# Kernel tuning notes

Hardware: AMD Instinct MI355X
Metric: run time of the kernel (lower is better)

## Reference

```python
import jax, jax.numpy as jnp
import numpy as np

N = 200000      # nodes
E = 1600000     # edges
B = 1000        # graphs
SD = 64         # state_dim
AD = 32         # action_dim
H = 128         # HIDDEN_LAYER
EPS = 1e-5


def setup_inputs() -> dict:
    key = jax.random.key(0)
    ks = jax.random.split(key, 16)
    x = jax.random.normal(ks[0], (N, SD), dtype=jnp.float32)
    action = jax.random.normal(ks[1], (N, AD), dtype=jnp.float32)
    edge_index = jax.random.randint(ks[2], (2, E), 0, N, dtype=jnp.int64)
    batch_size = jnp.sort(jax.random.randint(ks[3], (N,), 0, B, dtype=jnp.int64))
    # parameters (Linear weights stored [in, out]; torch init std=0.1 for fc layers)
    W_gcn = jax.random.normal(ks[4], (SD, H), dtype=jnp.float32) / np.sqrt(SD)
    b_gcn = jnp.zeros((H,), jnp.float32)
    g0 = jnp.ones((H,), jnp.float32); be0 = jnp.zeros((H,), jnp.float32)
    W1 = jax.random.normal(ks[5], (H, H), dtype=jnp.float32) * 0.1
    b1 = jnp.zeros((H,), jnp.float32)
    g1 = jnp.ones((H,), jnp.float32); be1 = jnp.zeros((H,), jnp.float32)
    W2 = jax.random.normal(ks[6], (AD, H), dtype=jnp.float32) * 0.1
    b2 = jnp.zeros((H,), jnp.float32)
    g2 = jnp.ones((H,), jnp.float32); be2 = jnp.zeros((H,), jnp.float32)
    W3 = jax.random.normal(ks[7], (2 * H, 1), dtype=jnp.float32) * 0.1
    b3 = jnp.zeros((1,), jnp.float32)
    return dict(x=x, action=action, W_gcn=W_gcn, b_gcn=b_gcn, g0=g0, be0=be0,
                W1=W1, b1=b1, g1=g1, be1=be1, W2=W2, b2=b2, g2=g2, be2=be2,
                W3=W3, b3=b3, edge_index=edge_index, batch_size=batch_size)


def _bn(h, gamma, beta):
    # BatchNorm1d, training-mode batch statistics over the node axis
    mu = jnp.mean(h, axis=0)
    var = jnp.var(h, axis=0)
    return (h - mu) * jax.lax.rsqrt(var + EPS) * gamma + beta


def _gcn(x, edge_index, W, b):
    # GCN conv with self-loops and symmetric normalization:
    # out_i = sum_{j in N(i) u {i}} (d_i d_j)^{-1/2} (x_j W) + b
    loops = jnp.arange(N, dtype=edge_index.dtype)
    src = jnp.concatenate([edge_index[0], loops])
    dst = jnp.concatenate([edge_index[1], loops])
    deg = jax.ops.segment_sum(jnp.ones_like(dst, dtype=x.dtype), dst, num_segments=N)
    dinv = jax.lax.rsqrt(deg)                       # deg >= 1 due to self-loops
    norm = dinv[src] * dinv[dst]                    # [E+N]
    xw = x @ W                                      # [N, H]
    msg = xw[src] * norm[:, None]                   # [E+N, H]
    return jax.ops.segment_sum(msg, dst, num_segments=N) + b


def reference(x, action, W_gcn, b_gcn, g0, be0, W1, b1, g1, be1,
              W2, b2, g2, be2, W3, b3, edge_index, batch_size):
    h0 = jax.nn.relu(_gcn(x, edge_index, W_gcn, b_gcn))
    h0n = _bn(h0, g0, be0)
    h1 = jax.nn.relu(h0n @ W1 + b1)
    h1n = _bn(h1, g1, be1)
    h2 = jax.nn.relu(action @ W2 + b2)
    h2n = _bn(h2, g2, be2)
    feat = jnp.concatenate([h1n, h2n], axis=1)      # [N, 2H]
    sums = jax.ops.segment_sum(feat, batch_size, num_segments=B)
    cnts = jax.ops.segment_sum(jnp.ones((N,), feat.dtype), batch_size, num_segments=B)
    pooled = sums / jnp.maximum(cnts, 1.0)[:, None]  # [B, 2H]
    return pooled @ W3 + b3                          # [B, 1]
```

## Files before the change

kernel.cpp:

```cpp
#include <hip/hip_runtime.h>

typedef unsigned short u16;
typedef unsigned int   u32;
typedef __bf16 bf16x8 __attribute__((ext_vector_type(8)));
typedef float  f32x4  __attribute__((ext_vector_type(4)));

#define EPS 1e-5f
#define BSHIFT 9

__device__ __forceinline__ float b2f(u16 u){ union{u32 i; float f;} v; v.i=((u32)u)<<16; return v.f; }
__device__ __forceinline__ u16 f2b(float f){
  u32 x = __float_as_uint(f);
  u32 r = x + 0x7fffu + ((x>>16)&1u);
  return (u16)(r>>16);
}

template<int K, bool RELU, bool HASBIAS, bool AF32, bool POOL>
__global__ __launch_bounds__(256, 3) void k_gemm(const void* __restrict__ Av,
                                                 const u16* __restrict__ BhiT,
                                                 const u16* __restrict__ BloT,
                                                 const float* __restrict__ bias,
                                                 u16* __restrict__ C,
                                                 float* __restrict__ stats,
                                                 const int* __restrict__ batch,
                                                 float* __restrict__ P, int M)
{
  constexpr int KM = K / 8;
  constexpr int KR = K / 32;
  __shared__ u16 lds[2 * 64 * K];
  __shared__ float sred[64], qred[64];
  const int tid = threadIdx.x;
  const int ch = blockIdx.x & 1;
  for (int i = tid; i < 64 * KM; i += 256) {
    const int n = i / KM, kb = i % KM;
    const int kb2 = kb ^ (n & (KM - 1));
    const int gsrc = ((ch * 64 + n) * KM + kb) * 8;
    *(uint4*)(&lds[(n * KM + kb2) * 8])          = *(const uint4*)(BhiT + gsrc);
    *(uint4*)(&lds[64 * K + (n * KM + kb2) * 8]) = *(const uint4*)(BloT + gsrc);
  }
  if (tid < 64) { sred[tid] = 0.f; qred[tid] = 0.f; }
  __syncthreads();
  const int wid = tid >> 6, lane = tid & 63, q = lane >> 4, r16 = lane & 15;
  const int ntiles = M >> 6;
  const int t0 = blockIdx.x >> 1, tstride = gridDim.x >> 1;
  float ls[4], lq[4];
#pragma unroll
  for (int nb = 0; nb < 4; nb++) { ls[nb] = 0.f; lq[nb] = 0.f; }
  float bv[4];
#pragma unroll
  for (int nb = 0; nb < 4; nb++) bv[nb] = HASBIAS ? bias[ch * 64 + nb * 16 + r16] : 0.f;

  bf16x8 av[KR];
  bf16x8 avn[KR];
  f32x4  fx0[KR], fx1[KR];
  int bgc[4], bgn[4];

  auto issueA = [&](int tile) {
    const int arow = (tile << 6) + (wid << 4) + r16;
    if (AF32) {
      const float* Af = (const float*)Av + (size_t)arow * K + q * 8;
#pragma unroll
      for (int kk = 0; kk < KR; kk++) {
        fx0[kk] = *(const f32x4*)(Af + kk * 32);
        fx1[kk] = *(const f32x4*)(Af + kk * 32 + 4);
      }
    } else {
      const u16* Ab = (const u16*)Av + (size_t)arow * K + q * 8;
#pragma unroll
      for (int kk = 0; kk < KR; kk++) avn[kk] = *(const bf16x8*)(Ab + kk * 32);
    }
    if (POOL) {
      const int rbase = (tile << 6) + (wid << 4) + (q << 2);
#pragma unroll
      for (int r = 0; r < 4; r++) bgn[r] = batch[rbase + r];
    }
  };
  auto commitA = [&]() {
    if (AF32) {
#pragma unroll
      for (int kk = 0; kk < KR; kk++)
#pragma unroll
        for (int j = 0; j < 4; j++) { av[kk][j] = (__bf16)fx0[kk][j]; av[kk][4 + j] = (__bf16)fx1[kk][j]; }
    } else {
#pragma unroll
      for (int kk = 0; kk < KR; kk++) av[kk] = avn[kk];
    }
    if (POOL) {
#pragma unroll
      for (int r = 0; r < 4; r++) bgc[r] = bgn[r];
    }
  };

  if (t0 < ntiles) issueA(t0);
  for (int tile = t0; tile < ntiles; tile += tstride) {
    commitA();
    const int nxt = tile + tstride;
    if (nxt < ntiles) issueA(nxt);

    f32x4 acc[4];
#pragma unroll
    for (int nb = 0; nb < 4; nb++) acc[nb] = (f32x4){0.f, 0.f, 0.f, 0.f};
#pragma unroll
    for (int kk = 0; kk < KR; kk++) {
#pragma unroll
      for (int nb = 0; nb < 4; nb++) {
        const int n = nb * 16 + r16;
        const int kb2 = (kk * 4 + q) ^ (n & (KM - 1));
        const bf16x8 bh = *(const bf16x8*)(&lds[(n * KM + kb2) * 8]);
        const bf16x8 bl = *(const bf16x8*)(&lds[64 * K + (n * KM + kb2) * 8]);
        acc[nb] = __builtin_amdgcn_mfma_f32_16x16x32_bf16(av[kk], bh, acc[nb], 0, 0, 0);
        acc[nb] = __builtin_amdgcn_mfma_f32_16x16x32_bf16(av[kk], bl, acc[nb], 0, 0, 0);
      }
    }

    const int rbase = (tile << 6) + (wid << 4) + (q << 2);
#pragma unroll
    for (int nb = 0; nb < 4; nb++) {
      const int col = ch * 64 + nb * 16 + r16;
#pragma unroll
      for (int r = 0; r < 4; r++) {
        float v = acc[nb][r] + bv[nb];
        if (RELU) v = fmaxf(v, 0.f);
        ls[nb] += v; lq[nb] += v * v;
        if (!POOL) C[(size_t)(rbase + r) * 128 + col] = f2b(v);
        else acc[nb][r] = v;
      }
    }
    if (POOL) {
      const int g0 = __shfl(bgc[0], 0, 64);
      const int g1 = __shfl(bgc[3], 48, 64);
      for (int g = g0; g <= g1; ++g) {
#pragma unroll
        for (int nb = 0; nb < 4; nb++) {
          float sv = 0.f;
#pragma unroll
          for (int r = 0; r < 4; r++) sv += (bgc[r] == g) ? acc[nb][r] : 0.f;
          sv += __shfl_xor(sv, 16, 64);
          sv += __shfl_xor(sv, 32, 64);
          if (q == 0) atomicAdd(&P[g * 128 + ch * 64 + nb * 16 + r16], sv);
        }
      }
    }
  }
#pragma unroll
  for (int nb = 0; nb < 4; nb++) {
    atomicAdd(&sred[nb * 16 + r16], ls[nb]);
    atomicAdd(&qred[nb * 16 + r16], lq[nb]);
  }
  __syncthreads();
  if (tid < 64) {
    atomicAdd(&stats[ch * 64 + tid], sred[tid]);
    atomicAdd(&stats[128 + ch * 64 + tid], qred[tid]);
  }
}

__global__ void k_prep0(const float* __restrict__ Wg, const float* __restrict__ W2,
                        u16* __restrict__ WghiT, u16* __restrict__ WgloT,
                        u16* __restrict__ W2hiT, u16* __restrict__ W2loT,
                        const int* __restrict__ batch, int* __restrict__ gofs,
                        int* __restrict__ zbase, int zwords, int NZ, int N, int B)
{
  const int bid = blockIdx.x, t = threadIdx.x;
  if (bid < NZ) {
    const int i = bid * 2048 + t * 8;
    if (i < zwords) {
      *(int4*)(zbase + i)     = make_int4(0, 0, 0, 0);
      *(int4*)(zbase + i + 4) = make_int4(0, 0, 0, 0);
    }
  } else if (bid < NZ + 48) {
    const int i = (bid - NZ) * 256 + t;
    if (i < 64 * 128) {
      int k = i >> 7, n = i & 127;
      float w = Wg[i]; u16 h = f2b(w);
      WghiT[n * 64 + k] = h; WgloT[n * 64 + k] = f2b(w - b2f(h));
    } else if (i < 64 * 128 + 32 * 128) {
      int j = i - 64 * 128;
      int k = j >> 7, n = j & 127;
      float w = W2[j]; u16 h = f2b(w);
      W2hiT[n * 32 + k] = h; W2loT[n * 32 + k] = f2b(w - b2f(h));
    }
  } else {
    const int i = (bid - NZ - 48) * 256 + t;
    if (i == 0) { for (int g = 0; g <= batch[0]; g++) gofs[g] = 0; }
    if (i == N - 1) { for (int g = batch[N - 1] + 1; g <= B; g++) gofs[g] = N; }
    if (i < N - 1) {
      const int b0 = batch[i], b1 = batch[i + 1];
      for (int g = b0 + 1; g <= b1; g++) gofs[g] = i + 1;
    }
  }
}

__global__ __launch_bounds__(256) void k_bincnt(const int* __restrict__ dst, int* __restrict__ btot,
                                                int E, int NB)
{
  extern __shared__ int hist[];
  const int tid = threadIdx.x;
  for (int i = tid; i < NB; i += 256) hist[i] = 0;
  __syncthreads();
  const int chunk = (E + gridDim.x - 1) / gridDim.x;
  const int start = blockIdx.x * chunk;
  const int end = min(start + chunk, E);
  for (int e = start + tid; e < end; e += 256) atomicAdd(&hist[((u32)dst[e]) >> BSHIFT], 1);
  __syncthreads();
  for (int i = tid; i < NB; i += 256) if (hist[i]) atomicAdd(&btot[i], hist[i]);
}

__global__ void k_exscan(const int* __restrict__ in, int* __restrict__ out, int n)
{
  __shared__ int s[256];
  const int t = threadIdx.x;
  const int per = (n + 255) / 256;
  const int base = t * per;
  int loc[8]; int sum = 0;
  for (int j = 0; j < per; j++) { int v = (base + j < n) ? in[base + j] : 0; loc[j] = sum; sum += v; }
  s[t] = sum; __syncthreads();
  for (int o = 1; o < 256; o <<= 1) {
    int x = (t >= o) ? s[t - o] : 0;
    __syncthreads();
    s[t] += x;
    __syncthreads();
  }
  const int ex = s[t] - sum;
  for (int j = 0; j < per; j++) if (base + j < n) out[base + j] = ex + loc[j];
  if (t == 255) out[n] = s[255];
}

__global__ __launch_bounds__(256) void k_bin(const int* __restrict__ src, const int* __restrict__ dst,
                                             const int* __restrict__ bbase, int* __restrict__ bcur,
                                             uint2* __restrict__ pairs, int E, int NB)
{
  extern __shared__ int lds[];
  int* hist = lds; int* wbase = lds + NB;
  const int tid = threadIdx.x;
  for (int i = tid; i < NB; i += 256) hist[i] = 0;
  __syncthreads();
  const int chunk = (E + gridDim.x - 1) / gridDim.x;
  const int start = blockIdx.x * chunk;
  const int end = min(start + chunk, E);
  for (int e = start + tid; e < end; e += 256) atomicAdd(&hist[((u32)dst[e]) >> BSHIFT], 1);
  __syncthreads();
  for (int i = tid; i < NB; i += 256) {
    int c = hist[i];
    wbase[i] = c ? bbase[i] + atomicAdd(&bcur[i], c) : 0;
    hist[i] = 0;
  }
  __syncthreads();
  for (int e = start + tid; e < end; e += 256) {
    const int d = dst[e];
    const int b = ((u32)d) >> BSHIFT;
    const int o = atomicAdd(&hist[b], 1);
    pairs[wbase[b] + o] = make_uint2((u32)d, (u32)src[e]);
  }
}

__global__ __launch_bounds__(256) void k_bucket(const uint2* __restrict__ pairs,
                                                const int* __restrict__ bbase,
                                                const float* __restrict__ x,
                                                int* __restrict__ offsets, float* __restrict__ dinv,
                                                int* __restrict__ elist, u16* __restrict__ y,
                                                int N, int NB, int Etot)
{
  __shared__ int hist[512];
  __shared__ int scan[256];
  __shared__ int lcur[512];
  __shared__ float sdinv[512];
  const int b = blockIdx.x, t = threadIdx.x;
  const int nbase = b << BSHIFT;
  const int nn = min(1 << BSHIFT, N - nbase);
  hist[t] = 0; hist[256 + t] = 0;
  __syncthreads();
  const int p0 = bbase[b], p1 = bbase[b + 1];
  for (int p = p0 + t; p < p1; p += 256) atomicAdd(&hist[pairs[p].x - nbase], 1);
  __syncthreads();
  const int h0 = hist[2 * t], h1 = hist[2 * t + 1];
  const int psum = h0 + h1;
  scan[t] = psum; __syncthreads();
  for (int o = 1; o < 256; o <<= 1) {
    int xx = (t >= o) ? scan[t - o] : 0;
    __syncthreads();
    scan[t] += xx;
    __syncthreads();
  }
  const int ex = scan[t] - psum;
  const int li0 = 2 * t, li1 = 2 * t + 1;
  if (li0 < nn) {
    const int i = nbase + li0;
    const int off = p0 + ex + i;
    const float d = rsqrtf((float)(h0 + 1));
    offsets[i] = off; elist[off] = i; lcur[li0] = off + 1;
    dinv[i] = d; sdinv[li0] = d;
  }
  if (li1 < nn) {
    const int i = nbase + li1;
    const int off = p0 + ex + h0 + i;
    const float d = rsqrtf((float)(h1 + 1));
    offsets[i] = off; elist[off] = i; lcur[li1] = off + 1;
    dinv[i] = d; sdinv[li1] = d;
  }
  if (b == NB - 1 && t == 0) offsets[N] = Etot;
  __syncthreads();
  for (int p = p0 + t; p < p1; p += 256) {
    const uint2 pr = pairs[p];
    const int pos = atomicAdd(&lcur[pr.x - nbase], 1);
    elist[pos] = (int)pr.y;
  }
  const size_t ebase = (size_t)nbase * 64;
  const int total = nn * 64;
  for (int i = t * 8; i < total; i += 256 * 8) {
    const float d = sdinv[i >> 6];
    f32x4 a = *(const f32x4*)(x + ebase + i);
    f32x4 c = *(const f32x4*)(x + ebase + i + 4);
    u16 o[8];
#pragma unroll
    for (int j = 0; j < 4; j++) { o[j] = f2b(a[j] * d); o[4 + j] = f2b(c[j] * d); }
    *(uint4*)(y + ebase + i) = *(uint4*)o;
  }
}

__global__ __launch_bounds__(256) void k_agg(const u16* __restrict__ y, const int* __restrict__ offsets,
                                             const int* __restrict__ elist, const float* __restrict__ dinv,
                                             u16* __restrict__ aggx, int n)
{
  const int lane = threadIdx.x & 63;
  const int half = lane >> 5, l32 = lane & 31;
  const int g4 = l32 >> 3, sub = lane & 7;
  const int wid  = (blockIdx.x * 256 + threadIdx.x) >> 6;
  const int nw   = gridDim.x * 4;
  const int npair = (n + 1) >> 1;
  for (int pr = wid; pr < npair; pr += nw) {
    const int node = pr * 2 + half;
    const int s0 = offsets[node], s1 = offsets[node + 1];
    const int mydeg = s1 - s0;
    const int degA = __shfl(mydeg, 0, 64);
    const int degB = __shfl(mydeg, 32, 64);
    const int degmax = max(degA, degB);
    float a[8];
#pragma unroll
    for (int t = 0; t < 8; t++) a[t] = 0.f;
    for (int base = 0; base < degmax; base += 32) {
      const int m = mydeg - base;
      const int ev = (base + l32 < mydeg) ? elist[s0 + base + l32] : 0;
      const int iters = (min(32, degmax - base) + 3) >> 2;
      for (int it = 0; it < iters; it++) {
        const int j = it * 4 + g4;
        const int idx = __shfl(ev, half * 32 + j, 64);
        if (j < m) {
          const uint4 v = *(const uint4*)(y + (size_t)idx * 64 + sub * 8);
          const u32 w[4] = {v.x, v.y, v.z, v.w};
#pragma unroll
          for (int t = 0; t < 4; t++) {
            a[2 * t]     += b2f((u16)w[t]);
            a[2 * t + 1] += b2f((u16)(w[t] >> 16));
          }
        }
      }
    }
#pragma unroll
    for (int t = 0; t < 8; t++) {
      a[t] += __shfl_xor(a[t], 8, 64);
      a[t] += __shfl_xor(a[t], 16, 64);
    }
    if (g4 == 0) {
      const float di = dinv[node];
      u16 o[8];
#pragma unroll
      for (int t = 0; t < 8; t++) o[t] = f2b(a[t] * di);
      *(uint4*)(aggx + (size_t)node * 64 + sub * 8) = *(uint4*)o;
    }
  }
}

__global__ void k_prep1(const float* __restrict__ stats0, const float* __restrict__ W1,
                        const float* __restrict__ b1, const float* __restrict__ g0,
                        const float* __restrict__ be0, u16* __restrict__ W1hiT,
                        u16* __restrict__ W1loT, float* __restrict__ b1p, float n)
{
  __shared__ float A[8], Csh[8];
  const int t = threadIdx.x;
  if (t < 8) {
    const int k = blockIdx.x * 8 + t;
    const float mu = stats0[k] / n;
    const float var = fmaxf(stats0[128 + k] / n - mu * mu, 0.f);
    const float a = g0[k] * rsqrtf(var + EPS);
    A[t] = a; Csh[t] = be0[k] - mu * a;
  }
  __syncthreads();
  float acc = (blockIdx.x == 0) ? b1[t] : 0.f;
#pragma unroll
  for (int kk = 0; kk < 8; kk++) {
    const int k = blockIdx.x * 8 + kk;
    const float w0 = W1[k * 128 + t];
    acc += Csh[kk] * w0;
    const float w = A[kk] * w0;
    const u16 h = f2b(w);
    W1hiT[t * 128 + k] = h;
    W1loT[t * 128 + k] = f2b(w - b2f(h));
  }
  atomicAdd(&b1p[t], acc);
}

__global__ void k_prep2(const float* __restrict__ stats1, const float* __restrict__ stats2,
                        const float* __restrict__ g1, const float* __restrict__ be1,
                        const float* __restrict__ g2, const float* __restrict__ be2,
                        const float* __restrict__ W3, const float* __restrict__ b3,
                        float* __restrict__ w1f, float* __restrict__ w2f,
                        float* __restrict__ constS, float n)
{
  __shared__ float red[256];
  const int t = threadIdx.x;
  float c, wv;
  if (t < 128) {
    const float mu = stats1[t] / n;
    const float var = fmaxf(stats1[128 + t] / n - mu * mu, 0.f);
    const float a = g1[t] * rsqrtf(var + EPS);
    c = be1[t] - mu * a;
    wv = W3[t];
    w1f[t] = a * wv;
  } else {
    const int f = t - 128;
    const float mu = stats2[f] / n;
    const float var = fmaxf(stats2[128 + f] / n - mu * mu, 0.f);
    const float a = g2[f] * rsqrtf(var + EPS);
    c = be2[f] - mu * a;
    wv = W3[t];
    w2f[f] = a * wv;
  }
  red[t] = c * wv; __syncthreads();
  for (int o = 128; o; o >>= 1) { if (t < o) red[t] += red[t + o]; __syncthreads(); }
  if (t == 0) { constS[0] = red[0] + b3[0]; constS[1] = b3[0]; }
}

__global__ void k_out2(const float* __restrict__ P1, const float* __restrict__ P2,
                       const int* __restrict__ gofs, const float* __restrict__ w1f,
                       const float* __restrict__ w2f, const float* __restrict__ constS,
                       float* __restrict__ out, int B)
{
  const int lane = threadIdx.x & 63;
  const int g = (blockIdx.x * 256 + threadIdx.x) >> 6;
  if (g >= B) return;
  const int c = gofs[g + 1] - gofs[g];
  const int k = 2 * lane;
  float d = P1[g * 128 + k] * w1f[k] + P1[g * 128 + k + 1] * w1f[k + 1]
          + P2[g * 128 + k] * w2f[k] + P2[g * 128 + k + 1] * w2f[k + 1];
#pragma unroll
  for (int o = 1; o < 64; o <<= 1) d += __shfl_xor(d, o, 64);
  if (lane == 0) out[g] = (c > 0) ? d / (float)c + constS[0] : constS[1];
}

extern "C" void kernel_launch(void* const* d_in, const int* in_sizes, int n_in,
                              void* d_out, int out_size, void* d_ws, size_t ws_size,
                              hipStream_t stream)
{
  const float* x    = (const float*)d_in[0];
  const float* act  = (const float*)d_in[1];
  const float* Wg   = (const float*)d_in[2];
  const float* bg   = (const float*)d_in[3];
  const float* g0   = (const float*)d_in[4];
  const float* be0  = (const float*)d_in[5];
  const float* W1   = (const float*)d_in[6];
  const float* b1   = (const float*)d_in[7];
  const float* g1   = (const float*)d_in[8];
  const float* be1  = (const float*)d_in[9];
  const float* W2   = (const float*)d_in[10];
  const float* b2   = (const float*)d_in[11];
  const float* g2   = (const float*)d_in[12];
  const float* be2  = (const float*)d_in[13];
  const float* W3   = (const float*)d_in[14];
  const float* b3   = (const float*)d_in[15];
  const int* eidx   = (const int*)d_in[16];
  const int* batch  = (const int*)d_in[17];

  const int N = in_sizes[17];
  const int E = in_sizes[16] / 2;
  const int B = out_size;
  const int* src = eidx;
  const int* dst = eidx + E;
  const int NB = (N + (1 << BSHIFT) - 1) >> BSHIFT;

  char* ws = (char*)d_ws;
  size_t off = 0;
  auto alloc = [&](size_t bytes) -> char* {
    off = (off + 255) & ~(size_t)255;
    char* p = ws + off; off += bytes; return p;
  };

  u16* bufA = (u16*)alloc((size_t)N * 128 * 2);
  u16* xb   = (u16*)alloc((size_t)N * 64 * 2);
  u16* aggx = (u16*)alloc((size_t)N * 64 * 2);

  int zwords = 768 + 128 + 2 * NB + 2 * 128 * B;
  zwords = (zwords + 7) & ~7;
  char* zbase   = alloc((size_t)zwords * 4);
  float* stats0 = (float*)zbase;
  float* stats1 = stats0 + 256;
  float* stats2 = stats1 + 256;
  float* b1p    = stats2 + 256;
  int*   btot   = (int*)(b1p + 128);
  int*   bcur   = btot + NB;
  float* P1     = (float*)(bcur + NB);
  float* P2     = P1 + 128 * B;

  int*   offsets = (int*)alloc((size_t)(N + 1) * 4);
  float* dinv    = (float*)alloc((size_t)N * 4);
  int*   elist   = (int*)alloc((size_t)(E + N) * 4);
  uint2* pairs   = (uint2*)alloc((size_t)E * 8);
  int*   bbase   = (int*)alloc((size_t)(NB + 1) * 4);
  int*   gofs    = (int*)alloc((size_t)(B + 1) * 4);
  u16*   WghiT   = (u16*)alloc(128 * 64 * 2);
  u16*   WgloT   = (u16*)alloc(128 * 64 * 2);
  u16*   W1hiT   = (u16*)alloc(128 * 128 * 2);
  u16*   W1loT   = (u16*)alloc(128 * 128 * 2);
  u16*   W2hiT   = (u16*)alloc(128 * 32 * 2);
  u16*   W2loT   = (u16*)alloc(128 * 32 * 2);
  float* w1f     = (float*)alloc(128 * 4);
  float* w2f     = (float*)alloc(128 * 4);
  float* constS  = (float*)alloc(2 * 4);

  u16* h0 = bufA;

  const int NZ = (zwords + 2047) / 2048;
  const int nbounds = (N + 255) / 256;
  k_prep0<<<NZ + 48 + nbounds, 256, 0, stream>>>(Wg, W2, WghiT, WgloT, W2hiT, W2loT,
                                                 batch, gofs, (int*)zbase, zwords, NZ, N, B);
  k_bincnt<<<256, 256, NB * 4, stream>>>(dst, btot, E, NB);
  k_exscan<<<1, 256, 0, stream>>>(btot, bbase, NB);
  k_bin<<<256, 256, 2 * NB * 4, stream>>>(src, dst, bbase, bcur, pairs, E, NB);
  k_bucket<<<NB, 256, 0, stream>>>(pairs, bbase, x, offsets, dinv, elist, xb, N, NB, E + N);
  k_agg<<<2048, 256, 0, stream>>>(xb, offsets, elist, dinv, aggx, N);
  k_gemm<64, true, true, false, false><<<768, 256, 0, stream>>>(aggx, WghiT, WgloT, bg,
                                                                h0, stats0, nullptr, nullptr, N);
  k_prep1<<<16, 128, 0, stream>>>(stats0, W1, b1, g0, be0, W1hiT, W1loT, b1p, (float)N);
  k_gemm<128, true, true, false, true><<<768, 256, 0, stream>>>(h0, W1hiT, W1loT, b1p,
                                                                nullptr, stats1, batch, P1, N);
  k_gemm<32, true, true, true, true><<<768, 256, 0, stream>>>(act, W2hiT, W2loT, b2,
                                                              nullptr, stats2, batch, P2, N);
  k_prep2<<<1, 256, 0, stream>>>(stats1, stats2, g1, be1, g2, be2, W3, b3, w1f, w2f, constS, (float)N);
  k_out2<<<(B * 64 + 255) / 256, 256, 0, stream>>>(P1, P2, gofs, w1f, w2f, constS, (float*)d_out, B);
}
```

Baseline: 394.3 us.

## Drop register prefetch of A tiles and raise GEMM occupancy target

Removes the software double-buffering of the A operand and batch ids, so each tile is loaded and used directly. This frees registers, and launch bounds rise from 3 to 4 blocks per SIMD. Blocks are now split into contiguous halves by output column chunk instead of interleaving even and odd block indices. The bet is that higher occupancy hides memory latency better than explicit prefetching did, at the risk of exposed load latency per tile.

```diff
diff --git a/kernel.cpp b/kernel.cpp
--- a/kernel.cpp
+++ b/kernel.cpp
@@ -16,7 +16,7 @@
 }
 
 template<int K, bool RELU, bool HASBIAS, bool AF32, bool POOL>
-__global__ __launch_bounds__(256, 3) void k_gemm(const void* __restrict__ Av,
+__global__ __launch_bounds__(256, 4) void k_gemm(const void* __restrict__ Av,
                                                  const u16* __restrict__ BhiT,
                                                  const u16* __restrict__ BloT,
                                                  const float* __restrict__ bias,
@@ -30,7 +30,9 @@
   __shared__ u16 lds[2 * 64 * K];
   __shared__ float sred[64], qred[64];
   const int tid = threadIdx.x;
-  const int ch = blockIdx.x & 1;
+  const int halfg = gridDim.x >> 1;
+  const int ch = (blockIdx.x >= halfg) ? 1 : 0;
+  const int t0 = blockIdx.x - ch * halfg;
   for (int i = tid; i < 64 * KM; i += 256) {
     const int n = i / KM, kb = i % KM;
     const int kb2 = kb ^ (n & (KM - 1));
@@ -42,7 +44,6 @@
   __syncthreads();
   const int wid = tid >> 6, lane = tid & 63, q = lane >> 4, r16 = lane & 15;
   const int ntiles = M >> 6;
-  const int t0 = blockIdx.x >> 1, tstride = gridDim.x >> 1;
   float ls[4], lq[4];
 #pragma unroll
   for (int nb = 0; nb < 4; nb++) { ls[nb] = 0.f; lq[nb] = 0.f; }
@@ -50,52 +51,23 @@
 #pragma unroll
   for (int nb = 0; nb < 4; nb++) bv[nb] = HASBIAS ? bias[ch * 64 + nb * 16 + r16] : 0.f;
 
-  bf16x8 av[KR];
-  bf16x8 avn[KR];
-  f32x4  fx0[KR], fx1[KR];
-  int bgc[4], bgn[4];
-
-  auto issueA = [&](int tile) {
+  for (int tile = t0; tile < ntiles; tile += halfg) {
     const int arow = (tile << 6) + (wid << 4) + r16;
+    bf16x8 av[KR];
     if (AF32) {
       const float* Af = (const float*)Av + (size_t)arow * K + q * 8;
 #pragma unroll
       for (int kk = 0; kk < KR; kk++) {
-        fx0[kk] = *(const f32x4*)(Af + kk * 32);
-        fx1[kk] = *(const f32x4*)(Af + kk * 32 + 4);
+        f32x4 x0 = *(const f32x4*)(Af + kk * 32);
+        f32x4 x1 = *(const f32x4*)(Af + kk * 32 + 4);
+#pragma unroll
+        for (int j = 0; j < 4; j++) { av[kk][j] = (__bf16)x0[j]; av[kk][4 + j] = (__bf16)x1[j]; }
       }
     } else {
       const u16* Ab = (const u16*)Av + (size_t)arow * K + q * 8;
 #pragma unroll
-      for (int kk = 0; kk < KR; kk++) avn[kk] = *(const bf16x8*)(Ab + kk * 32);
-    }
-    if (POOL) {
-      const int rbase = (tile << 6) + (wid << 4) + (q << 2);
-#pragma unroll
-      for (int r = 0; r < 4; r++) bgn[r] = batch[rbase + r];
-    }
-  };
-  auto commitA = [&]() {
-    if (AF32) {
-#pragma unroll
-      for (int kk = 0; kk < KR; kk++)
-#pragma unroll
-        for (int j = 0; j < 4; j++) { av[kk][j] = (__bf16)fx0[kk][j]; av[kk][4 + j] = (__bf16)fx1[kk][j]; }
-    } else {
-#pragma unroll
-      for (int kk = 0; kk < KR; kk++) av[kk] = avn[kk];
-    }
-    if (POOL) {
-#pragma unroll
-      for (int r = 0; r < 4; r++) bgc[r] = bgn[r];
-    }
-  };
-
-  if (t0 < ntiles) issueA(t0);
-  for (int tile = t0; tile < ntiles; tile += tstride) {
-    commitA();
-    const int nxt = tile + tstride;
-    if (nxt < ntiles) issueA(nxt);
+      for (int kk = 0; kk < KR; kk++) av[kk] = *(const bf16x8*)(Ab + kk * 32);
+    }
 
     f32x4 acc[4];
 #pragma unroll
@@ -127,14 +99,17 @@
       }
     }
     if (POOL) {
-      const int g0 = __shfl(bgc[0], 0, 64);
-      const int g1 = __shfl(bgc[3], 48, 64);
+      int bg[4];
+#pragma unroll
+      for (int r = 0; r < 4; r++) bg[r] = batch[rbase + r];
+      const int g0 = __shfl(bg[0], 0, 64);
+      const int g1 = __shfl(bg[3], 48, 64);
       for (int g = g0; g <= g1; ++g) {
 #pragma unroll
         for (int nb = 0; nb < 4; nb++) {
           float sv = 0.f;
 #pragma unroll
-          for (int r = 0; r < 4; r++) sv += (bgc[r] == g) ? acc[nb][r] : 0.f;
+          for (int r = 0; r < 4; r++) sv += (bg[r] == g) ? acc[nb][r] : 0.f;
           sv += __shfl_xor(sv, 16, 64);
           sv += __shfl_xor(sv, 32, 64);
           if (q == 0) atomicAdd(&P[g * 128 + ch * 64 + nb * 16 + r16], sv);
```

Result: slower. 409.4 us (+3.8%).
